# Optimization experiments

Hardware: AMD Instinct MI355X
Metric: run time of the kernel (lower is better)

## Reference

```python
import jax, jax.numpy as jnp
import numpy as np

CH = 50        # channel
RED = 2        # reduction -> match channels = 25
KS = 3         # ksize
SM_SCALE = 10.0
SCALES = [1.0, 0.9, 0.8, 0.7, 0.6]
ESCAPE_NAN = 1e-4


def prelu(x, a):
    return jnp.where(x >= 0, x, a * x)


def conv1x1(x, w, b):
    # x: [B,Ci,H,W], w: [Co,Ci], b: [Co]
    return jnp.einsum('bihw,oi->bohw', x, w) + b[None, :, None, None]


def patches3(x):
    # extract 3x3 stride-1 SAME patches, torch-unfold (C,kh,kw) ordering
    # x: [B,C,H,W] -> [B, H*W, C, 3, 3]
    B, C, H, W = x.shape
    p = jnp.pad(x, ((0, 0), (0, 0), (1, 1), (1, 1)))
    cols = jnp.stack([p[:, :, i:i + H, j:j + W]
                      for i in range(KS) for j in range(KS)], axis=2)  # [B,C,9,H,W]
    cols = cols.reshape(B, C, KS, KS, H * W)
    return cols.transpose(0, 4, 1, 2, 3)


def setup_inputs() -> dict:
    key = jax.random.key(0)
    ks = jax.random.split(key, 7)
    B, H, W = 4, 48, 48
    f = CH // RED  # 25
    s1 = 1.0 / np.sqrt(CH)
    return {
        'x': jax.random.normal(ks[0], (B, CH, H, W), jnp.float32),
        # conv_match_L_base: 1x1 conv CH->f + PReLU
        'w_base': jax.random.normal(ks[1], (f, CH), jnp.float32) * s1,
        'b_base': jnp.zeros((f,), jnp.float32),
        'a_base': jnp.float32(0.25),
        # conv_match: 1x1 conv CH->f + PReLU
        'w_match': jax.random.normal(ks[2], (f, CH), jnp.float32) * s1,
        'b_match': jnp.zeros((f,), jnp.float32),
        'a_match': jnp.float32(0.25),
        # conv_assembly: 1x1 conv CH->CH + PReLU
        'w_asm': jax.random.normal(ks[3], (CH, CH), jnp.float32) * s1,
        'b_asm': jnp.zeros((CH,), jnp.float32),
        'a_asm': jnp.float32(0.25),
    }


def reference(x, w_base, b_base, a_base, w_match, b_match, a_match,
              w_asm, b_asm, a_asm):
    B, C, H, W = x.shape
    match_base = prelu(conv1x1(x, w_base, b_base), a_base)  # [B,25,H,W]

    w_list, raw_list = [], []
    for s in SCALES:
        if s == 1.0:
            ref = x
        else:
            Hs, Ws = int(H * s), int(W * s)
            ref = jax.image.resize(x, (B, C, Hs, Ws), method='cubic')
        base = prelu(conv1x1(ref, w_asm, b_asm), a_asm)       # [B,C,Hs,Ws]
        raw_list.append(patches3(base))                       # [B,Hs*Ws,C,3,3]
        refm = prelu(conv1x1(ref, w_match, b_match), a_match)  # [B,25,Hs,Ws]
        w_list.append(patches3(refm))                         # [B,Hs*Ws,25,3,3]

    wi = jnp.concatenate(w_list, axis=1)    # [B, L, 25, 3, 3]
    raw = jnp.concatenate(raw_list, axis=1)  # [B, L, C, 3, 3]

    def attend(xb, wb, rb):
        # xb: [25,H,W]; wb: [L,25,3,3]; rb: [L,C,3,3]
        norm = jnp.maximum(
            jnp.sqrt(jnp.sum(wb * wb, axis=(1, 2, 3), keepdims=True)),
            ESCAPE_NAN)
        wn = wb / norm
        score = jax.lax.conv_general_dilated(
            xb[None], wn, (1, 1), [(1, 1), (1, 1)])[0]        # [L,H,W]
        attn = jax.nn.softmax(score * SM_SCALE, axis=0)
        # conv_transpose2d(stride=1, pad=1) == corr with flipped, transposed kernel
        wt = jnp.flip(rb, axis=(2, 3)).transpose(1, 0, 2, 3)  # [C,L,3,3]
        out = jax.lax.conv_general_dilated(
            attn[None], wt, (1, 1), [(1, 1), (1, 1)])[0]      # [C,H,W]
        return out * 0.25

    y = jax.vmap(attend)(match_base, wi, raw)
    return y + x  # res_scale = 1
```

## Files before the change

kernel.cpp:

```cpp
#include <hip/hip_runtime.h>
#include <hip/hip_bf16.h>
#include <math.h>


#define L_TOT 7470
#define L_PAD 7680
#define NCHUNK 4
#define CHUNK_TILES 30
#define KD    256
#define JD    512
#define HW    2304

typedef unsigned short u16;
typedef __attribute__((ext_vector_type(8))) short bf16x8;
typedef __attribute__((ext_vector_type(4))) float f32x4;

__device__ inline u16 f2b(float f) {
    __hip_bfloat16 h = __float2bfloat16(f);
    return __builtin_bit_cast(u16, h);
}
__device__ inline float b2f(u16 u) {
    __hip_bfloat16 h = __builtin_bit_cast(__hip_bfloat16, u);
    return __bfloat162float(h);
}

__constant__ int c_hs[5]   = {48, 43, 38, 33, 28};
__constant__ int c_loff[6] = {0, 2304, 4153, 5597, 6686, 7470};

__device__ inline void decode_l(int l, int& si, int& hs, int& pos) {
    si = 0;
#pragma unroll
    for (int s = 0; s < 4; ++s)
        if (l >= c_loff[s + 1]) si = s + 1;
    pos = l - c_loff[si];
    hs = c_hs[si];
}

#define GLOAD16(g, l) __builtin_amdgcn_global_load_lds(                          \
        (__attribute__((address_space(1))) const void*)(g),                      \
        (__attribute__((address_space(3))) void*)(l), 16, 0, 0)

__global__ void resize_weights_kernel(float* __restrict__ wmall) {
    int r = blockIdx.x * blockDim.x + threadIdx.x;
    if (r >= 142) return;
    int sizes[4] = {43, 38, 33, 28};
    int si = 0, i = r, woffs = 0;
    for (si = 0; si < 4; ++si) {
        if (i < sizes[si]) break;
        i -= sizes[si];
        woffs += sizes[si] * 48;
    }
    int osz = sizes[si];
    float inv_scale = 48.0f / (float)osz;
    float kscale = inv_scale;
    float sample_f = ((float)i + 0.5f) * inv_scale - 0.5f;
    float w[48];
    float tot = 0.f;
    for (int j = 0; j < 48; ++j) {
        float t = fabsf(sample_f - (float)j) / kscale;
        float v;
        if (t >= 2.f)       v = 0.f;
        else if (t >= 1.f)  v = ((-0.5f * t + 2.5f) * t - 4.f) * t + 2.f;
        else                v = ((1.5f * t - 2.5f) * t) * t + 1.f;
        w[j] = v;
        tot += v;
    }
    float invt = 1.f / tot;
    for (int j = 0; j < 48; ++j) wmall[woffs + i * 48 + j] = w[j] * invt;
}

__global__ void resize_h(const float* __restrict__ in, const float* __restrict__ wm,
                         float* __restrict__ tmp, int osz) {
    int idx = blockIdx.x * 256 + threadIdx.x;
    int total = 200 * osz * 48;
    if (idx >= total) return;
    int xi = idx % 48;
    int t = idx / 48;
    int yo = t % osz;
    int bc = t / osz;
    const float* wr = wm + yo * 48;
    const float* ip = in + (size_t)bc * 2304 + xi;
    float s = 0.f;
#pragma unroll
    for (int yi = 0; yi < 48; ++yi) s += wr[yi] * ip[yi * 48];
    tmp[idx] = s;
}

__global__ void resize_w(const float* __restrict__ tmp, const float* __restrict__ wm,
                         float* __restrict__ refout, int osz) {
    int idx = blockIdx.x * 256 + threadIdx.x;
    int total = 200 * osz * osz;
    if (idx >= total) return;
    int xo = idx % osz;
    int t = idx / osz;
    int yo = t % osz;
    int bc = t / osz;
    const float* wr = wm + xo * 48;
    const float* ip = tmp + ((size_t)bc * osz + yo) * 48;
    float s = 0.f;
#pragma unroll
    for (int xi = 0; xi < 48; ++xi) s += wr[xi] * ip[xi];
    refout[idx] = s;
}

__global__ void conv1x1_prelu(const float* __restrict__ in, const float* __restrict__ w,
                              const float* __restrict__ bias, const float* __restrict__ a,
                              float* __restrict__ outp, int P, int Co) {
    int idx = blockIdx.x * 256 + threadIdx.x;
    int total = 4 * Co * P;
    if (idx >= total) return;
    int p = idx % P;
    int t = idx / P;
    int co = t % Co;
    int b = t / Co;
    const float* ip = in + (size_t)b * 50 * P + p;
    const float* wr = w + co * 50;
    float s = bias[co];
#pragma unroll
    for (int ci = 0; ci < 50; ++ci) s += wr[ci] * ip[(size_t)ci * P];
    float av = a[0];
    outp[idx] = (s >= 0.f) ? s : av * s;
}

__global__ void q_build(const float* __restrict__ mb, u16* __restrict__ Q) {
    int idx = blockIdx.x * 256 + threadIdx.x;
    if (idx >= 4 * HW * KD) return;
    int k = idx % KD;
    int t = idx / KD;
    int p = t % HW;
    int b = t / HW;
    float v = 0.f;
    if (k < 225) {
        int c = k / 9, r = k % 9, ky = r / 3, kx = r % 3;
        int y = p / 48, xx = p % 48;
        int yy = y + ky - 1, xv = xx + kx - 1;
        if (yy >= 0 && yy < 48 && xv >= 0 && xv < 48)
            v = mb[((size_t)(b * 25 + c)) * HW + yy * 48 + xv];
    }
    Q[idx] = f2b(v);
}

__global__ void norms_kernel(const float* __restrict__ refm_all, float* __restrict__ norms) {
    int idx = blockIdx.x * 256 + threadIdx.x;
    if (idx >= 4 * L_TOT) return;
    int l = idx % L_TOT;
    int b = idx / L_TOT;
    int si, hs, pos;
    decode_l(l, si, hs, pos);
    int P = hs * hs;
    int ly = pos / hs, lx = pos % hs;
    const float* rb = refm_all + (size_t)100 * c_loff[si] + (size_t)(b * 25) * P;
    float ss = 0.f;
    for (int c = 0; c < 25; ++c) {
        const float* rc = rb + (size_t)c * P;
#pragma unroll
        for (int ky = 0; ky < 3; ++ky) {
#pragma unroll
            for (int kx = 0; kx < 3; ++kx) {
                int yy = ly + ky - 1, xv = lx + kx - 1;
                if (yy >= 0 && yy < hs && xv >= 0 && xv < hs) {
                    float v = rc[yy * hs + xv];
                    ss += v * v;
                }
            }
        }
    }
    norms[idx] = 10.0f / fmaxf(sqrtf(ss), 1e-4f);
}

__global__ void kt_build(const float* __restrict__ refm_all, const float* __restrict__ norms,
                         u16* __restrict__ K) {
    int idx = blockIdx.x * 256 + threadIdx.x;
    if (idx >= 4 * L_PAD * KD) return;
    int k = idx % KD;
    int t = idx / KD;
    int l = t % L_PAD;
    int b = t / L_PAD;
    float v = 0.f;
    if (k < 225 && l < L_TOT) {
        int si, hs, pos;
        decode_l(l, si, hs, pos);
        int P = hs * hs;
        int ly = pos / hs, lx = pos % hs;
        int c = k / 9, r = k % 9, ky = r / 3, kx = r % 3;
        int yy = ly + ky - 1, xv = lx + kx - 1;
        if (yy >= 0 && yy < hs && xv >= 0 && xv < hs)
            v = refm_all[(size_t)100 * c_loff[si] + ((size_t)(b * 25 + c)) * P + yy * hs + xv]
                * norms[(size_t)b * L_TOT + l];
    }
    K[idx] = f2b(v);
}

__global__ void v_build(const float* __restrict__ base_all, u16* __restrict__ VT) {
    int idx = blockIdx.x * 256 + threadIdx.x;
    if (idx >= 4 * JD * L_PAD) return;
    int l = idx % L_PAD;
    int t = idx / L_PAD;
    int j = t % JD;
    int b = t / JD;
    float v = 0.f;
    if (j < 450 && l < L_TOT) {
        int si, hs, pos;
        decode_l(l, si, hs, pos);
        int P = hs * hs;
        int ly = pos / hs, lx = pos % hs;
        int c = j / 9, r = j % 9, ky = r / 3, kx = r % 3;
        int yy = ly + ky - 1, xv = lx + kx - 1;
        if (yy >= 0 && yy < hs && xv >= 0 && xv < hs)
            v = base_all[(size_t)200 * c_loff[si] + ((size_t)(b * 50 + c)) * P + yy * hs + xv];
    }
    VT[idx] = f2b(v);
}

__global__ __launch_bounds__(256, 4) void attn_score(
    const u16* __restrict__ Qg, const u16* __restrict__ Kg,
    u16* __restrict__ Ag, float* __restrict__ mC, float* __restrict__ dC) {
    __shared__ u16 smem[64 * KD];
    __shared__ float sm_m[2][64], sm_d[2][64];
    const int bx = blockIdx.x, by = blockIdx.y;
    const int mt = by % 36, zq = by / 36;
    const int z16 = bx + 8 * zq;
    const int b = z16 >> 2, chunk = z16 & 3;
    const int bm = mt * 64;
    const u16* Q = Qg + (size_t)b * HW * KD;
    const u16* K = Kg + (size_t)b * L_PAD * KD;
    u16* A = Ag + (size_t)b * HW * L_PAD;
    const int tid = threadIdx.x, lane = tid & 63, wid = tid >> 6;
    const int wr = wid >> 1, wc = wid & 1;
    const int l15 = lane & 15, l16 = lane >> 4;
    const int l7 = lane & 7;
    const int r_lo = lane >> 5;
    const int u_dst = lane & 31;

    {
        const u16* qrow = Q + (size_t)(bm + wid * 16 + r_lo) * KD;
        u16* qdst = smem + (size_t)(wid * 16) * KD;
#pragma unroll
        for (int q = 0; q < 8; ++q) {
            int sw = (u_dst ^ ((q * 2 + r_lo) & 7)) * 8;
            GLOAD16(qrow + (size_t)(q * 2) * KD + sw, qdst + (q * 2) * KD);
        }
    }
    __syncthreads();
    bf16x8 qf[2][8];
#pragma unroll
    for (int m = 0; m < 2; ++m)
#pragma unroll
        for (int k = 0; k < 8; ++k)
            qf[m][k] = *(const bf16x8*)&smem[(size_t)(wr * 32 + m * 16 + l15) * KD
                                             + (((k * 4 + l16) ^ l7) * 8)];
    __syncthreads();

    float mrun[2][4];
#pragma unroll
    for (int m = 0; m < 2; ++m)
#pragma unroll
        for (int r = 0; r < 4; ++r) mrun[m][r] = -3e38f;

    const int t0 = chunk * CHUNK_TILES;
    const int colb_base = wc * 32 + l15;

    for (int t = t0; t < t0 + CHUNK_TILES; ++t) {
        {
            const u16* krow = K + (size_t)(t * 64 + wid * 16 + r_lo) * KD;
            u16* kdst = smem + (size_t)(wid * 16) * KD;
#pragma unroll
            for (int q = 0; q < 8; ++q) {
                int sw = (u_dst ^ ((q * 2 + r_lo) & 7)) * 8;
                GLOAD16(krow + (size_t)(q * 2) * KD + sw, kdst + (q * 2) * KD);
            }
        }
        __syncthreads();
        f32x4 acc[2][2];
#pragma unroll
        for (int m = 0; m < 2; ++m)
#pragma unroll
            for (int n = 0; n < 2; ++n) acc[m][n] = (f32x4){0.f, 0.f, 0.f, 0.f};
#pragma unroll
        for (int k = 0; k < 8; ++k) {
            bf16x8 bfr[2];
#pragma unroll
            for (int n = 0; n < 2; ++n)
                bfr[n] = *(const bf16x8*)&smem[(size_t)(wc * 32 + n * 16 + l15) * KD
                                               + (((k * 4 + l16) ^ l7) * 8)];
#pragma unroll
            for (int m = 0; m < 2; ++m)
#pragma unroll
                for (int n = 0; n < 2; ++n)
                    acc[m][n] = __builtin_amdgcn_mfma_f32_16x16x32_bf16(qf[m][k], bfr[n], acc[m][n], 0, 0, 0);
        }
        const int col0 = t * 64 + colb_base;
        const bool v0 = col0 < L_TOT, v1 = col0 + 16 < L_TOT;
#pragma unroll
        for (int m = 0; m < 2; ++m)
#pragma unroll
            for (int r = 0; r < 4; ++r) {
                float s0 = v0 ? acc[m][0][r] : -3e38f;
                float s1 = v1 ? acc[m][1][r] : -3e38f;
                mrun[m][r] = fmaxf(mrun[m][r], fmaxf(s0, s1));
            }
        __syncthreads();
    }

#pragma unroll
    for (int m = 0; m < 2; ++m)
#pragma unroll
        for (int r = 0; r < 4; ++r) {
            float mv = mrun[m][r];
#pragma unroll
            for (int st = 1; st <= 8; st <<= 1)
                mv = fmaxf(mv, __shfl_xor(mv, st));
            mrun[m][r] = mv;
        }
    if (l15 == 0) {
#pragma unroll
        for (int m = 0; m < 2; ++m)
#pragma unroll
            for (int r = 0; r < 4; ++r)
                sm_m[wc][wr * 32 + m * 16 + l16 * 4 + r] = mrun[m][r];
    }
    __syncthreads();
#pragma unroll
    for (int m = 0; m < 2; ++m)
#pragma unroll
        for (int r = 0; r < 4; ++r) {
            int row = wr * 32 + m * 16 + l16 * 4 + r;
            mrun[m][r] = fmaxf(sm_m[0][row], sm_m[1][row]);
        }

    float drun[2][4];
#pragma unroll
    for (int m = 0; m < 2; ++m)
#pragma unroll
        for (int r = 0; r < 4; ++r) drun[m][r] = 0.f;

    for (int t = t0; t < t0 + CHUNK_TILES; ++t) {
        {
            const u16* krow = K + (size_t)(t * 64 + wid * 16 + r_lo) * KD;
            u16* kdst = smem + (size_t)(wid * 16) * KD;
#pragma unroll
            for (int q = 0; q < 8; ++q) {
                int sw = (u_dst ^ ((q * 2 + r_lo) & 7)) * 8;
                GLOAD16(krow + (size_t)(q * 2) * KD + sw, kdst + (q * 2) * KD);
            }
        }
        __syncthreads();
        f32x4 acc[2][2];
#pragma unroll
        for (int m = 0; m < 2; ++m)
#pragma unroll
            for (int n = 0; n < 2; ++n) acc[m][n] = (f32x4){0.f, 0.f, 0.f, 0.f};
#pragma unroll
        for (int k = 0; k < 8; ++k) {
            bf16x8 bfr[2];
#pragma unroll
            for (int n = 0; n < 2; ++n)
                bfr[n] = *(const bf16x8*)&smem[(size_t)(wc * 32 + n * 16 + l15) * KD
                                               + (((k * 4 + l16) ^ l7) * 8)];
#pragma unroll
            for (int m = 0; m < 2; ++m)
#pragma unroll
                for (int n = 0; n < 2; ++n)
                    acc[m][n] = __builtin_amdgcn_mfma_f32_16x16x32_bf16(qf[m][k], bfr[n], acc[m][n], 0, 0, 0);
        }
        const int col0 = t * 64 + colb_base;
#pragma unroll
        for (int m = 0; m < 2; ++m) {
            const int row = bm + wr * 32 + m * 16 + l16 * 4;
#pragma unroll
            for (int n = 0; n < 2; ++n) {
                const int col = col0 + n * 16;
                const bool vld = col < L_TOT;
#pragma unroll
                for (int r = 0; r < 4; ++r) {
                    float w = vld ? __expf(acc[m][n][r] - mrun[m][r]) : 0.f;
                    drun[m][r] += w;
                    A[(size_t)(row + r) * L_PAD + col] = f2b(w);
                }
            }
        }
        __syncthreads();
    }

#pragma unroll
    for (int m = 0; m < 2; ++m)
#pragma unroll
        for (int r = 0; r < 4; ++r) {
            float dv = drun[m][r];
#pragma unroll
            for (int st = 1; st <= 8; st <<= 1)
                dv += __shfl_xor(dv, st);
            drun[m][r] = dv;
        }
    if (l15 == 0) {
#pragma unroll
        for (int m = 0; m < 2; ++m)
#pragma unroll
            for (int r = 0; r < 4; ++r)
                sm_d[wc][wr * 32 + m * 16 + l16 * 4 + r] = drun[m][r];
    }
    __syncthreads();
    if (wc == 0 && l15 == 0) {
#pragma unroll
        for (int m = 0; m < 2; ++m)
#pragma unroll
            for (int r = 0; r < 4; ++r) {
                int row = wr * 32 + m * 16 + l16 * 4 + r;
                size_t o = (size_t)(chunk * 4 + b) * HW + bm + row;
                mC[o] = mrun[m][r];
                dC[o] = sm_d[0][row] + sm_d[1][row];
            }
    }
}

__global__ void combine_stats(const float* __restrict__ mC, const float* __restrict__ dC,
                              float* __restrict__ fac) {
    int idx = blockIdx.x * 256 + threadIdx.x;
    if (idx >= 4 * HW) return;
    int b = idx / HW, p = idx % HW;
    float m[NCHUNK], d[NCHUNK];
#pragma unroll
    for (int c = 0; c < NCHUNK; ++c) {
        size_t o = (size_t)(c * 4 + b) * HW + p;
        m[c] = mC[o]; d[c] = dC[o];
    }
    float mf = m[0];
#pragma unroll
    for (int c = 1; c < NCHUNK; ++c) mf = fmaxf(mf, m[c]);
    float w[NCHUNK], df = 0.f;
#pragma unroll
    for (int c = 0; c < NCHUNK; ++c) { w[c] = __expf(m[c] - mf); df += d[c] * w[c]; }
    float inv = 1.0f / df;
#pragma unroll
    for (int c = 0; c < NCHUNK; ++c) fac[(size_t)(c * 4 + b) * HW + p] = w[c] * inv;
}

__global__ __launch_bounds__(256) void gemm2_kernel(
    const u16* __restrict__ VT0, const u16* __restrict__ A0, u16* __restrict__ C0) {
    __shared__ u16 As[128 * 64];
    __shared__ u16 Bs[128 * 64];
    const int bx = blockIdx.x, by = blockIdx.y;
    const int within = by % 72, zq = by / 72;
    const int mt = within & 3, nt = within >> 2;
    const int z = bx + 8 * zq;
    const int batch = z >> 2, chunk = z & 3;
    const u16* A = VT0 + (size_t)batch * JD * L_PAD + chunk * (CHUNK_TILES * 64);
    const u16* B = A0 + (size_t)batch * HW * L_PAD + chunk * (CHUNK_TILES * 64);
    u16* C = C0 + (size_t)z * JD * HW;
    const int bm = mt * 128, bn = nt * 128;
    const int tid = threadIdx.x, lane = tid & 63, wid = tid >> 6;
    const int wr = wid >> 1, wc = wid & 1;
    const int srow = lane >> 3;
    const int scol = (lane & 7) * 8;

    f32x4 acc[4][4];
#pragma unroll
    for (int i = 0; i < 4; ++i)
#pragma unroll
        for (int j = 0; j < 4; ++j) acc[i][j] = (f32x4){0.f, 0.f, 0.f, 0.f};

    const u16* aG = A + (size_t)(bm + wid * 32 + srow) * L_PAD + scol;
    const u16* bG = B + (size_t)(bn + wid * 32 + srow) * L_PAD + scol;
    u16* aL = As + wid * 32 * 64;
    u16* bL = Bs + wid * 32 * 64;

    for (int t = 0; t < CHUNK_TILES; ++t) {
#pragma unroll
        for (int q = 0; q < 4; ++q) {
            GLOAD16(aG + (size_t)q * 8 * L_PAD, aL + q * 8 * 64);
            GLOAD16(bG + (size_t)q * 8 * L_PAD, bL + q * 8 * 64);
        }
        aG += 64;
        bG += 64;
        __syncthreads();
#pragma unroll
        for (int kc = 0; kc < 64; kc += 32) {
            bf16x8 af[4], bf[4];
#pragma unroll
            for (int m = 0; m < 4; ++m)
                af[m] = *(const bf16x8*)&As[(wr * 64 + m * 16 + (lane & 15)) * 64 + kc + (lane >> 4) * 8];
#pragma unroll
            for (int n = 0; n < 4; ++n)
                bf[n] = *(const bf16x8*)&Bs[(wc * 64 + n * 16 + (lane & 15)) * 64 + kc + (lane >> 4) * 8];
#pragma unroll
            for (int m = 0; m < 4; ++m)
#pragma unroll
                for (int n = 0; n < 4; ++n)
                    acc[m][n] = __builtin_amdgcn_mfma_f32_16x16x32_bf16(af[m], bf[n], acc[m][n], 0, 0, 0);
        }
        __syncthreads();
    }
    const int crow0 = bm + wr * 64 + (lane >> 4) * 4;
    const int ccol = bn + wc * 64 + (lane & 15);
#pragma unroll
    for (int m = 0; m < 4; ++m)
#pragma unroll
        for (int n = 0; n < 4; ++n)
#pragma unroll
            for (int r = 0; r < 4; ++r)
                C[(size_t)(crow0 + m * 16 + r) * HW + ccol + n * 16] = f2b(acc[m][n][r]);
}

__global__ void chunk_reduce(const u16* __restrict__ Zt, const float* __restrict__ fac,
                             u16* __restrict__ Zred) {
    int idx = blockIdx.x * 256 + threadIdx.x;
    int total = 4 * JD * HW / 8;
    if (idx >= total) return;
    int e8 = idx * 8;
    int pp = e8 % HW;
    int row = e8 / HW;
    int b = row / JD;
    float s[8] = {};
#pragma unroll
    for (int ch = 0; ch < NCHUNK; ++ch) {
        const float* fp = fac + (size_t)(ch * 4 + b) * HW + pp;
        bf16x8 zv = *(const bf16x8*)&Zt[((size_t)(b * 4 + ch) * JD + (row % JD)) * HW + pp];
#pragma unroll
        for (int u = 0; u < 8; ++u)
            s[u] += fp[u] * b2f((u16)zv[u]);
    }
    bf16x8 o;
#pragma unroll
    for (int u = 0; u < 8; ++u) o[u] = (short)f2b(s[u]);
    *(bf16x8*)&Zred[(size_t)row * HW + pp] = o;
}

__global__ void final_kernel(const u16* __restrict__ Zred, const float* __restrict__ x,
                             float* __restrict__ out) {
    int idx = blockIdx.x * 256 + threadIdx.x;
    if (idx >= 4 * 50 * HW) return;
    int p = idx % HW;
    int t = idx / HW;
    int c = t % 50;
    int b = t / 50;
    int y = p / 48, xx = p % 48;
    const u16* Zb = Zred + (size_t)b * JD * HW;
    float s = 0.f;
#pragma unroll
    for (int ky = 0; ky < 3; ++ky) {
        int yy = y + ky - 1;
        if (yy < 0 || yy >= 48) continue;
#pragma unroll
        for (int kx = 0; kx < 3; ++kx) {
            int xv = xx + kx - 1;
            if (xv < 0 || xv >= 48) continue;
            int pp = yy * 48 + xv;
            int j = c * 9 + (2 - ky) * 3 + (2 - kx);
            s += b2f(Zb[(size_t)j * HW + pp]);
        }
    }
    size_t o = ((size_t)b * 50 + c) * HW + p;
    out[o] = x[o] + 0.25f * s;
}

extern "C" void kernel_launch(void* const* d_in, const int* in_sizes, int n_in,
                              void* d_out, int out_size, void* d_ws, size_t ws_size,
                              hipStream_t stream) {
    const float* x       = (const float*)d_in[0];
    const float* w_base  = (const float*)d_in[1];
    const float* b_base  = (const float*)d_in[2];
    const float* a_base  = (const float*)d_in[3];
    const float* w_match = (const float*)d_in[4];
    const float* b_match = (const float*)d_in[5];
    const float* a_match = (const float*)d_in[6];
    const float* w_asm   = (const float*)d_in[7];
    const float* b_asm   = (const float*)d_in[8];
    const float* a_asm   = (const float*)d_in[9];
    float* out = (float*)d_out;
    float* ws = (float*)d_ws;
    (void)in_sizes; (void)n_in; (void)out_size; (void)ws_size;

    const int hs[5] = {48, 43, 38, 33, 28};
    const int loff[6] = {0, 2304, 4153, 5597, 6686, 7470};

    size_t off = 0;
    auto alloc = [&](size_t n) { size_t o = off; off += (n + 63) & ~(size_t)63; return o; };
    size_t o_wm = alloc(142 * 48);
    size_t o_rtmp = alloc((size_t)200 * 43 * 48);
    size_t o_ref[5];
    o_ref[0] = 0;
    for (int si = 1; si < 5; ++si) o_ref[si] = alloc((size_t)200 * hs[si] * hs[si]);
    size_t o_base = alloc((size_t)200 * L_TOT);
    size_t o_refm = alloc((size_t)100 * L_TOT);
    size_t o_mb = alloc((size_t)100 * HW);
    size_t o_norms = alloc((size_t)4 * L_TOT);

    size_t o_A = 0;
    size_t o_Q = (size_t)4 * HW * L_PAD / 2;
    size_t o_K = o_Q + (size_t)4 * HW * KD / 2;
    size_t o_VT = o_K + (size_t)4 * L_PAD * KD / 2;
    size_t o_Z = o_VT + (size_t)4 * JD * L_PAD / 2;
    size_t o_mc = o_Z + (size_t)16 * JD * HW / 2;
    size_t o_dc = o_mc + (size_t)16 * HW;
    size_t o_fac = o_dc + (size_t)16 * HW;
    size_t o_zred = o_fac + (size_t)16 * HW;

    u16* Qb = (u16*)(ws + o_Q);
    u16* Kb = (u16*)(ws + o_K);
    u16* VTb = (u16*)(ws + o_VT);
    u16* Ab = (u16*)(ws + o_A);
    u16* Zb = (u16*)(ws + o_Z);
    u16* Zrb = (u16*)(ws + o_zred);

    resize_weights_kernel<<<1, 256, 0, stream>>>(ws + o_wm);
    const int woff[5] = {0, 0, 43 * 48, (43 + 38) * 48, (43 + 38 + 33) * 48};
    for (int si = 1; si < 5; ++si) {
        int osz = hs[si];
        int n1 = 200 * osz * 48;
        resize_h<<<(n1 + 255) / 256, 256, 0, stream>>>(x, ws + o_wm + woff[si], ws + o_rtmp, osz);
        int n2 = 200 * osz * osz;
        resize_w<<<(n2 + 255) / 256, 256, 0, stream>>>(ws + o_rtmp, ws + o_wm + woff[si],
                                                       ws + o_ref[si], osz);
    }
    for (int si = 0; si < 5; ++si) {
        int P = hs[si] * hs[si];
        const float* in = (si == 0) ? x : ws + o_ref[si];
        int nb = 4 * 50 * P;
        conv1x1_prelu<<<(nb + 255) / 256, 256, 0, stream>>>(
            in, w_asm, b_asm, a_asm, ws + o_base + (size_t)200 * loff[si], P, 50);
        int nm = 4 * 25 * P;
        conv1x1_prelu<<<(nm + 255) / 256, 256, 0, stream>>>(
            in, w_match, b_match, a_match, ws + o_refm + (size_t)100 * loff[si], P, 25);
    }
    {
        int nmb = 4 * 25 * HW;
        conv1x1_prelu<<<(nmb + 255) / 256, 256, 0, stream>>>(x, w_base, b_base, a_base,
                                                             ws + o_mb, HW, 25);
    }
    {
        int n = 4 * HW * KD;
        q_build<<<(n + 255) / 256, 256, 0, stream>>>(ws + o_mb, Qb);
    }
    {
        int n = 4 * L_TOT;
        norms_kernel<<<(n + 255) / 256, 256, 0, stream>>>(ws + o_refm, ws + o_norms);
    }
    {
        int n = 4 * L_PAD * KD;
        kt_build<<<(n + 255) / 256, 256, 0, stream>>>(ws + o_refm, ws + o_norms, Kb);
    }
    {
        int n = 4 * JD * L_PAD;
        v_build<<<(n + 255) / 256, 256, 0, stream>>>(ws + o_base, VTb);
    }

    {
        dim3 g(8, 72, 1);
        attn_score<<<g, 256, 0, stream>>>(Qb, Kb, Ab, ws + o_mc, ws + o_dc);
    }
    combine_stats<<<(4 * HW + 255) / 256, 256, 0, stream>>>(ws + o_mc, ws + o_dc, ws + o_fac);

    {
        dim3 g(8, 144, 1);
        gemm2_kernel<<<g, 256, 0, stream>>>(VTb, Ab, Zb);
    }
    {
        int n = 4 * JD * HW / 8;
        chunk_reduce<<<(n + 255) / 256, 256, 0, stream>>>(Zb, ws + o_fac, Zrb);
    }
    final_kernel<<<(4 * 50 * HW + 255) / 256, 256, 0, stream>>>(Zrb, x, out);
}
```

Before: 558.7 us.

## Merge preprocessing launches and restructure Q/K/V packing with a decode table

Collapses the per-scale resize and conv1x1 launches into single fused kernels (resize_h_all, resize_w_all, conv_all), cutting roughly twenty small launches to a few. A precomputed decode table replaces the per-element scale search. q_build and kt_build now have each thread write nine taps for one channel instead of one element. v_build writes eight bf16 values per thread with a vector store. This targets launch overhead and redundant index math in the preprocessing phase, at the cost of more branching and some uncoalesced scalar stores in the Q/K builders.

New measurement: 534.1 us. 1.05x faster.

```diff
diff --git a/kernel.cpp b/kernel.cpp
--- a/kernel.cpp
+++ b/kernel.cpp
@@ -27,134 +27,224 @@
 __constant__ int c_hs[5]   = {48, 43, 38, 33, 28};
 __constant__ int c_loff[6] = {0, 2304, 4153, 5597, 6686, 7470};
 
-__device__ inline void decode_l(int l, int& si, int& hs, int& pos) {
-    si = 0;
-#pragma unroll
-    for (int s = 0; s < 4; ++s)
-        if (l >= c_loff[s + 1]) si = s + 1;
-    pos = l - c_loff[si];
-    hs = c_hs[si];
-}
-
 #define GLOAD16(g, l) __builtin_amdgcn_global_load_lds(                          \
         (__attribute__((address_space(1))) const void*)(g),                      \
         (__attribute__((address_space(3))) void*)(l), 16, 0, 0)
 
-__global__ void resize_weights_kernel(float* __restrict__ wmall) {
-    int r = blockIdx.x * blockDim.x + threadIdx.x;
-    if (r >= 142) return;
-    int sizes[4] = {43, 38, 33, 28};
-    int si = 0, i = r, woffs = 0;
-    for (si = 0; si < 4; ++si) {
-        if (i < sizes[si]) break;
-        i -= sizes[si];
-        woffs += sizes[si] * 48;
-    }
-    int osz = sizes[si];
-    float inv_scale = 48.0f / (float)osz;
-    float kscale = inv_scale;
-    float sample_f = ((float)i + 0.5f) * inv_scale - 0.5f;
-    float w[48];
-    float tot = 0.f;
-    for (int j = 0; j < 48; ++j) {
-        float t = fabsf(sample_f - (float)j) / kscale;
-        float v;
-        if (t >= 2.f)       v = 0.f;
-        else if (t >= 1.f)  v = ((-0.5f * t + 2.5f) * t - 4.f) * t + 2.f;
-        else                v = ((1.5f * t - 2.5f) * t) * t + 1.f;
-        w[j] = v;
-        tot += v;
-    }
-    float invt = 1.f / tot;
-    for (int j = 0; j < 48; ++j) wmall[woffs + i * 48 + j] = w[j] * invt;
-}
-
-__global__ void resize_h(const float* __restrict__ in, const float* __restrict__ wm,
-                         float* __restrict__ tmp, int osz) {
-    int idx = blockIdx.x * 256 + threadIdx.x;
-    int total = 200 * osz * 48;
-    if (idx >= total) return;
-    int xi = idx % 48;
-    int t = idx / 48;
+__global__ void prep_kernel(float* __restrict__ wmall, int* __restrict__ dtab) {
+    int r = blockIdx.x * 256 + threadIdx.x;
+    if (r < 142) {
+        int sizes[4] = {43, 38, 33, 28};
+        int si = 0, i = r, woffs = 0;
+        for (si = 0; si < 4; ++si) {
+            if (i < sizes[si]) break;
+            i -= sizes[si];
+            woffs += sizes[si] * 48;
+        }
+        int osz = sizes[si];
+        float inv_scale = 48.0f / (float)osz;
+        float kscale = inv_scale;
+        float sample_f = ((float)i + 0.5f) * inv_scale - 0.5f;
+        float w[48];
+        float tot = 0.f;
+        for (int j = 0; j < 48; ++j) {
+            float t = fabsf(sample_f - (float)j) / kscale;
+            float v;
+            if (t >= 2.f)       v = 0.f;
+            else if (t >= 1.f)  v = ((-0.5f * t + 2.5f) * t - 4.f) * t + 2.f;
+            else                v = ((1.5f * t - 2.5f) * t) * t + 1.f;
+            w[j] = v;
+            tot += v;
+        }
+        float invt = 1.f / tot;
+        for (int j = 0; j < 48; ++j) wmall[woffs + i * 48 + j] = w[j] * invt;
+    }
+    if (r < L_PAD) {
+        int v;
+        if (r >= L_TOT) v = (int)0x80000000u;
+        else {
+            int si = 0;
+#pragma unroll
+            for (int s = 0; s < 4; ++s)
+                if (r >= c_loff[s + 1]) si = s + 1;
+            int pos = r - c_loff[si];
+            int hs = c_hs[si];
+            int ly = pos / hs, lx = pos % hs;
+            v = si | (ly << 4) | (lx << 10);
+        }
+        dtab[r] = v;
+    }
+}
+
+__global__ void resize_h_all(const float* __restrict__ in, const float* __restrict__ wm,
+                             float* __restrict__ t1, float* __restrict__ t2,
+                             float* __restrict__ t3, float* __restrict__ t4) {
+    int idx = blockIdx.x * 256 + threadIdx.x;
+    int rem = idx, osz, woffm;
+    float* tmp;
+    if (rem < 200 * 43 * 48) { osz = 43; tmp = t1; woffm = 0; }
+    else {
+        rem -= 200 * 43 * 48;
+        if (rem < 200 * 38 * 48) { osz = 38; tmp = t2; woffm = 43 * 48; }
+        else {
+            rem -= 200 * 38 * 48;
+            if (rem < 200 * 33 * 48) { osz = 33; tmp = t3; woffm = (43 + 38) * 48; }
+            else {
+                rem -= 200 * 33 * 48;
+                if (rem >= 200 * 28 * 48) return;
+                osz = 28; tmp = t4; woffm = (43 + 38 + 33) * 48;
+            }
+        }
+    }
+    int xi = rem % 48;
+    int t = rem / 48;
     int yo = t % osz;
     int bc = t / osz;
-    const float* wr = wm + yo * 48;
+    const float* wr = wm + (size_t)(woffm + yo * 48);
     const float* ip = in + (size_t)bc * 2304 + xi;
     float s = 0.f;
 #pragma unroll
     for (int yi = 0; yi < 48; ++yi) s += wr[yi] * ip[yi * 48];
-    tmp[idx] = s;
-}
-
-__global__ void resize_w(const float* __restrict__ tmp, const float* __restrict__ wm,
-                         float* __restrict__ refout, int osz) {
-    int idx = blockIdx.x * 256 + threadIdx.x;
-    int total = 200 * osz * osz;
-    if (idx >= total) return;
-    int xo = idx % osz;
-    int t = idx / osz;
+    tmp[rem] = s;
+}
+
+__global__ void resize_w_all(const float* __restrict__ t1, const float* __restrict__ t2,
+                             const float* __restrict__ t3, const float* __restrict__ t4,
+                             const float* __restrict__ wm,
+                             float* __restrict__ r1, float* __restrict__ r2,
+                             float* __restrict__ r3, float* __restrict__ r4) {
+    int idx = blockIdx.x * 256 + threadIdx.x;
+    int rem = idx, osz, woffm;
+    const float* tmp;
+    float* outp;
+    if (rem < 200 * 43 * 43) { osz = 43; tmp = t1; outp = r1; woffm = 0; }
+    else {
+        rem -= 200 * 43 * 43;
+        if (rem < 200 * 38 * 38) { osz = 38; tmp = t2; outp = r2; woffm = 43 * 48; }
+        else {
+            rem -= 200 * 38 * 38;
+            if (rem < 200 * 33 * 33) { osz = 33; tmp = t3; outp = r3; woffm = (43 + 38) * 48; }
+            else {
+                rem -= 200 * 33 * 33;
+                if (rem >= 200 * 28 * 28) return;
+                osz = 28; tmp = t4; outp = r4; woffm = (43 + 38 + 33) * 48;
+            }
+        }
+    }
+    int xo = rem % osz;
+    int t = rem / osz;
     int yo = t % osz;
     int bc = t / osz;
-    const float* wr = wm + xo * 48;
+    const float* wr = wm + (size_t)(woffm + xo * 48);
     const float* ip = tmp + ((size_t)bc * osz + yo) * 48;
     float s = 0.f;
 #pragma unroll
     for (int xi = 0; xi < 48; ++xi) s += wr[xi] * ip[xi];
-    refout[idx] = s;
-}
-
-__global__ void conv1x1_prelu(const float* __restrict__ in, const float* __restrict__ w,
-                              const float* __restrict__ bias, const float* __restrict__ a,
-                              float* __restrict__ outp, int P, int Co) {
-    int idx = blockIdx.x * 256 + threadIdx.x;
-    int total = 4 * Co * P;
-    if (idx >= total) return;
-    int p = idx % P;
-    int t = idx / P;
-    int co = t % Co;
-    int b = t / Co;
+    outp[rem] = s;
+}
+
+__global__ void conv_all(const float* __restrict__ x,
+                         const float* __restrict__ r1, const float* __restrict__ r2,
+                         const float* __restrict__ r3, const float* __restrict__ r4,
+                         const float* __restrict__ w_asm, const float* __restrict__ b_asm,
+                         const float* __restrict__ a_asm,
+                         const float* __restrict__ w_match, const float* __restrict__ b_match,
+                         const float* __restrict__ a_match,
+                         const float* __restrict__ w_base, const float* __restrict__ b_base,
+                         const float* __restrict__ a_base,
+                         float* __restrict__ base_out, float* __restrict__ refm_out,
+                         float* __restrict__ mb_out) {
+    int idx = blockIdx.x * 256 + threadIdx.x;
+    int rem = idx, P, loffv, NCO;
+    const float* in;
+    if (rem < 400 * 2304) { P = 2304; in = x; loffv = 0; NCO = 100; }
+    else {
+        rem -= 400 * 2304;
+        if (rem < 300 * 1849) { P = 1849; in = r1; loffv = 2304; NCO = 75; }
+        else {
+            rem -= 300 * 1849;
+            if (rem < 300 * 1444) { P = 1444; in = r2; loffv = 4153; NCO = 75; }
+            else {
+                rem -= 300 * 1444;
+                if (rem < 300 * 1089) { P = 1089; in = r3; loffv = 5597; NCO = 75; }
+                else {
+                    rem -= 300 * 1089;
+                    if (rem >= 300 * 784) return;
+                    P = 784; in = r4; loffv = 6686; NCO = 75;
+                }
+            }
+        }
+    }
+    int p = rem % P;
+    int t = rem / P;
+    int co = t % NCO;
+    int b = t / NCO;
     const float* ip = in + (size_t)b * 50 * P + p;
-    const float* wr = w + co * 50;
-    float s = bias[co];
+    const float* wr;
+    float bias, av;
+    float* outp;
+    if (co < 50) {
+        wr = w_asm + co * 50; bias = b_asm[co]; av = a_asm[0];
+        outp = base_out + (size_t)200 * loffv + ((size_t)(b * 50 + co)) * P + p;
+    } else if (co < 75) {
+        int cm = co - 50;
+        wr = w_match + cm * 50; bias = b_match[cm]; av = a_match[0];
+        outp = refm_out + (size_t)100 * loffv + ((size_t)(b * 25 + cm)) * P + p;
+    } else {
+        int cm = co - 75;
+        wr = w_base + cm * 50; bias = b_base[cm]; av = a_base[0];
+        outp = mb_out + ((size_t)(b * 25 + cm)) * P + p;
+    }
+    float s = bias;
 #pragma unroll
     for (int ci = 0; ci < 50; ++ci) s += wr[ci] * ip[(size_t)ci * P];
-    float av = a[0];
-    outp[idx] = (s >= 0.f) ? s : av * s;
+    *outp = (s >= 0.f) ? s : av * s;
 }
 
 __global__ void q_build(const float* __restrict__ mb, u16* __restrict__ Q) {
     int idx = blockIdx.x * 256 + threadIdx.x;
-    if (idx >= 4 * HW * KD) return;
-    int k = idx % KD;
-    int t = idx / KD;
+    if (idx >= 4 * HW * 25) return;
+    int c = idx % 25;
+    int t = idx / 25;
     int p = t % HW;
     int b = t / HW;
-    float v = 0.f;
-    if (k < 225) {
-        int c = k / 9, r = k % 9, ky = r / 3, kx = r % 3;
-        int y = p / 48, xx = p % 48;
-        int yy = y + ky - 1, xv = xx + kx - 1;
-        if (yy >= 0 && yy < 48 && xv >= 0 && xv < 48)
-            v = mb[((size_t)(b * 25 + c)) * HW + yy * 48 + xv];
-    }
-    Q[idx] = f2b(v);
-}
-
-__global__ void norms_kernel(const float* __restrict__ refm_all, float* __restrict__ norms) {
-    int idx = blockIdx.x * 256 + threadIdx.x;
-    if (idx >= 4 * L_TOT) return;
-    int l = idx % L_TOT;
-    int b = idx / L_TOT;
-    int si, hs, pos;
-    decode_l(l, si, hs, pos);
-    int P = hs * hs;
-    int ly = pos / hs, lx = pos % hs;
+    int y = p / 48, xx = p % 48;
+    const float* rc = mb + (size_t)(b * 25 + c) * HW;
+    u16 ov[9];
+#pragma unroll
+    for (int ky = 0; ky < 3; ++ky)
+#pragma unroll
+        for (int kx = 0; kx < 3; ++kx) {
+            int yy = y + ky - 1, xv = xx + kx - 1;
+            float v = (yy >= 0 && yy < 48 && xv >= 0 && xv < 48) ? rc[yy * 48 + xv] : 0.f;
+            ov[ky * 3 + kx] = f2b(v);
+        }
+    u16* dst = Q + (size_t)(b * HW + p) * KD + c * 9;
+#pragma unroll
+    for (int r = 0; r < 9; ++r) dst[r] = ov[r];
+    if (c == 24) {
+        u16* z = dst + 9;
+#pragma unroll
+        for (int i = 0; i < 31; ++i) z[i] = 0;
+    }
+}
+
+__global__ void norms_kernel(const float* __restrict__ refm_all, const int* __restrict__ dtab,
+                             float* __restrict__ norms) {
+    int idx = blockIdx.x * 256 + threadIdx.x;
+    if (idx >= 4 * L_PAD) return;
+    int l = idx % L_PAD;
+    int b = idx / L_PAD;
+    int d = dtab[l];
+    if (d < 0) return;
+    int si = d & 15, ly = (d >> 4) & 63, lx = (d >> 10) & 63;
+    int hs = c_hs[si], P = hs * hs;
     const float* rb = refm_all + (size_t)100 * c_loff[si] + (size_t)(b * 25) * P;
     float ss = 0.f;
     for (int c = 0; c < 25; ++c) {
         const float* rc = rb + (size_t)c * P;
 #pragma unroll
-        for (int ky = 0; ky < 3; ++ky) {
+        for (int ky = 0; ky < 3; ++ky)
 #pragma unroll
             for (int kx = 0; kx < 3; ++kx) {
                 int yy = ly + ky - 1, xv = lx + kx - 1;
@@ -163,53 +253,71 @@
                     ss += v * v;
                 }
             }
-        }
-    }
-    norms[idx] = 10.0f / fmaxf(sqrtf(ss), 1e-4f);
-}
-
-__global__ void kt_build(const float* __restrict__ refm_all, const float* __restrict__ norms,
-                         u16* __restrict__ K) {
-    int idx = blockIdx.x * 256 + threadIdx.x;
-    if (idx >= 4 * L_PAD * KD) return;
-    int k = idx % KD;
-    int t = idx / KD;
+    }
+    norms[(size_t)b * L_PAD + l] = 10.0f / fmaxf(sqrtf(ss), 1e-4f);
+}
+
+__global__ void kt_build(const float* __restrict__ refm_all, const int* __restrict__ dtab,
+                         const float* __restrict__ norms, u16* __restrict__ K) {
+    int idx = blockIdx.x * 256 + threadIdx.x;
+    if (idx >= 4 * L_PAD * 25) return;
+    int c = idx % 25;
+    int t = idx / 25;
     int l = t % L_PAD;
     int b = t / L_PAD;
-    float v = 0.f;
-    if (k < 225 && l < L_TOT) {
-        int si, hs, pos;
-        decode_l(l, si, hs, pos);
-        int P = hs * hs;
-        int ly = pos / hs, lx = pos % hs;
-        int c = k / 9, r = k % 9, ky = r / 3, kx = r % 3;
-        int yy = ly + ky - 1, xv = lx + kx - 1;
-        if (yy >= 0 && yy < hs && xv >= 0 && xv < hs)
-            v = refm_all[(size_t)100 * c_loff[si] + ((size_t)(b * 25 + c)) * P + yy * hs + xv]
-                * norms[(size_t)b * L_TOT + l];
-    }
-    K[idx] = f2b(v);
-}
-
-__global__ void v_build(const float* __restrict__ base_all, u16* __restrict__ VT) {
-    int idx = blockIdx.x * 256 + threadIdx.x;
-    if (idx >= 4 * JD * L_PAD) return;
-    int l = idx % L_PAD;
-    int t = idx / L_PAD;
+    u16 ov[9] = {0, 0, 0, 0, 0, 0, 0, 0, 0};
+    int d = dtab[l];
+    if (d >= 0) {
+        int si = d & 15, ly = (d >> 4) & 63, lx = (d >> 10) & 63;
+        int hs = c_hs[si], P = hs * hs;
+        float nrm = norms[(size_t)b * L_PAD + l];
+        const float* rc = refm_all + (size_t)100 * c_loff[si] + (size_t)(b * 25 + c) * P;
+#pragma unroll
+        for (int ky = 0; ky < 3; ++ky)
+#pragma unroll
+            for (int kx = 0; kx < 3; ++kx) {
+                int yy = ly + ky - 1, xv = lx + kx - 1;
+                if (yy >= 0 && yy < hs && xv >= 0 && xv < hs)
+                    ov[ky * 3 + kx] = f2b(rc[yy * hs + xv] * nrm);
+            }
+    }
+    u16* dst = K + (size_t)(b * L_PAD + l) * KD + c * 9;
+#pragma unroll
+    for (int r = 0; r < 9; ++r) dst[r] = ov[r];
+    if (c == 24) {
+        u16* z = dst + 9;
+#pragma unroll
+        for (int i = 0; i < 31; ++i) z[i] = 0;
+    }
+}
+
+__global__ void v_build(const float* __restrict__ base_all, const int* __restrict__ dtab,
+                        u16* __restrict__ VT) {
+    int idx = blockIdx.x * 256 + threadIdx.x;
+    if (idx >= 4 * JD * (L_PAD / 8)) return;
+    int l8 = idx % (L_PAD / 8);
+    int t = idx / (L_PAD / 8);
     int j = t % JD;
     int b = t / JD;
-    float v = 0.f;
-    if (j < 450 && l < L_TOT) {
-        int si, hs, pos;
-        decode_l(l, si, hs, pos);
-        int P = hs * hs;
-        int ly = pos / hs, lx = pos % hs;
+    int l0 = l8 * 8;
+    bf16x8 ov = (bf16x8){0, 0, 0, 0, 0, 0, 0, 0};
+    if (j < 450) {
         int c = j / 9, r = j % 9, ky = r / 3, kx = r % 3;
-        int yy = ly + ky - 1, xv = lx + kx - 1;
-        if (yy >= 0 && yy < hs && xv >= 0 && xv < hs)
-            v = base_all[(size_t)200 * c_loff[si] + ((size_t)(b * 50 + c)) * P + yy * hs + xv];
-    }
-    VT[idx] = f2b(v);
+#pragma unroll
+        for (int u = 0; u < 8; ++u) {
+            int d = dtab[l0 + u];
+            float v = 0.f;
+            if (d >= 0) {
+                int si = d & 15, ly = (d >> 4) & 63, lx = (d >> 10) & 63;
+                int hs = c_hs[si], P = hs * hs;
+                int yy = ly + ky - 1, xv = lx + kx - 1;
+                if (yy >= 0 && yy < hs && xv >= 0 && xv < hs)
+                    v = base_all[(size_t)200 * c_loff[si] + (size_t)(b * 50 + c) * P + yy * hs + xv];
+            }
+            ov[u] = (short)f2b(v);
+        }
+    }
+    *(bf16x8*)&VT[(size_t)(b * JD + j) * L_PAD + l0] = ov;
 }
 
 __global__ __launch_bounds__(256, 4) void attn_score(
@@ -570,20 +678,22 @@
     float* ws = (float*)d_ws;
     (void)in_sizes; (void)n_in; (void)out_size; (void)ws_size;
 
-    const int hs[5] = {48, 43, 38, 33, 28};
-    const int loff[6] = {0, 2304, 4153, 5597, 6686, 7470};
-
     size_t off = 0;
     auto alloc = [&](size_t n) { size_t o = off; off += (n + 63) & ~(size_t)63; return o; };
     size_t o_wm = alloc(142 * 48);
-    size_t o_rtmp = alloc((size_t)200 * 43 * 48);
-    size_t o_ref[5];
-    o_ref[0] = 0;
-    for (int si = 1; si < 5; ++si) o_ref[si] = alloc((size_t)200 * hs[si] * hs[si]);
+    size_t o_dtab = alloc(L_PAD);
+    size_t o_t1 = alloc((size_t)200 * 43 * 48);
+    size_t o_t2 = alloc((size_t)200 * 38 * 48);
+    size_t o_t3 = alloc((size_t)200 * 33 * 48);
+    size_t o_t4 = alloc((size_t)200 * 28 * 48);
+    size_t o_r1 = alloc((size_t)200 * 43 * 43);
+    size_t o_r2 = alloc((size_t)200 * 38 * 38);
+    size_t o_r3 = alloc((size_t)200 * 33 * 33);
+    size_t o_r4 = alloc((size_t)200 * 28 * 28);
     size_t o_base = alloc((size_t)200 * L_TOT);
     size_t o_refm = alloc((size_t)100 * L_TOT);
     size_t o_mb = alloc((size_t)100 * HW);
-    size_t o_norms = alloc((size_t)4 * L_TOT);
+    size_t o_norms = alloc((size_t)4 * L_PAD);
 
     size_t o_A = 0;
     size_t o_Q = (size_t)4 * HW * L_PAD / 2;
@@ -601,47 +711,42 @@
     u16* Ab = (u16*)(ws + o_A);
     u16* Zb = (u16*)(ws + o_Z);
     u16* Zrb = (u16*)(ws + o_zred);
-
-    resize_weights_kernel<<<1, 256, 0, stream>>>(ws + o_wm);
-    const int woff[5] = {0, 0, 43 * 48, (43 + 38) * 48, (43 + 38 + 33) * 48};
-    for (int si = 1; si < 5; ++si) {
-        int osz = hs[si];
-        int n1 = 200 * osz * 48;
-        resize_h<<<(n1 + 255) / 256, 256, 0, stream>>>(x, ws + o_wm + woff[si], ws + o_rtmp, osz);
-        int n2 = 200 * osz * osz;
-        resize_w<<<(n2 + 255) / 256, 256, 0, stream>>>(ws + o_rtmp, ws + o_wm + woff[si],
-                                                       ws + o_ref[si], osz);
-    }
-    for (int si = 0; si < 5; ++si) {
-        int P = hs[si] * hs[si];
-        const float* in = (si == 0) ? x : ws + o_ref[si];
-        int nb = 4 * 50 * P;
-        conv1x1_prelu<<<(nb + 255) / 256, 256, 0, stream>>>(
-            in, w_asm, b_asm, a_asm, ws + o_base + (size_t)200 * loff[si], P, 50);
-        int nm = 4 * 25 * P;
-        conv1x1_prelu<<<(nm + 255) / 256, 256, 0, stream>>>(
-            in, w_match, b_match, a_match, ws + o_refm + (size_t)100 * loff[si], P, 25);
-    }
-    {
-        int nmb = 4 * 25 * HW;
-        conv1x1_prelu<<<(nmb + 255) / 256, 256, 0, stream>>>(x, w_base, b_base, a_base,
-                                                             ws + o_mb, HW, 25);
-    }
-    {
-        int n = 4 * HW * KD;
+    int* dtab = (int*)(ws + o_dtab);
+
+    prep_kernel<<<(L_PAD + 255) / 256, 256, 0, stream>>>(ws + o_wm, dtab);
+    {
+        int n = 200 * 48 * (43 + 38 + 33 + 28);
+        resize_h_all<<<(n + 255) / 256, 256, 0, stream>>>(x, ws + o_wm, ws + o_t1,
+                                                          ws + o_t2, ws + o_t3, ws + o_t4);
+    }
+    {
+        int n = 200 * (43 * 43 + 38 * 38 + 33 * 33 + 28 * 28);
+        resize_w_all<<<(n + 255) / 256, 256, 0, stream>>>(ws + o_t1, ws + o_t2, ws + o_t3,
+                                                          ws + o_t4, ws + o_wm, ws + o_r1,
+                                                          ws + o_r2, ws + o_r3, ws + o_r4);
+    }
+    {
+        int n = 400 * 2304 + 300 * (1849 + 1444 + 1089 + 784);
+        conv_all<<<(n + 255) / 256, 256, 0, stream>>>(
+            x, ws + o_r1, ws + o_r2, ws + o_r3, ws + o_r4,
+            w_asm, b_asm, a_asm, w_match, b_match, a_match, w_base, b_base, a_base,
+            ws + o_base, ws + o_refm, ws + o_mb);
+    }
+    {
+        int n = 4 * HW * 25;
         q_build<<<(n + 255) / 256, 256, 0, stream>>>(ws + o_mb, Qb);
     }
     {
-        int n = 4 * L_TOT;
-        norms_kernel<<<(n + 255) / 256, 256, 0, stream>>>(ws + o_refm, ws + o_norms);
-    }
-    {
-        int n = 4 * L_PAD * KD;
-        kt_build<<<(n + 255) / 256, 256, 0, stream>>>(ws + o_refm, ws + o_norms, Kb);
-    }
-    {
-        int n = 4 * JD * L_PAD;
-        v_build<<<(n + 255) / 256, 256, 0, stream>>>(ws + o_base, VTb);
+        int n = 4 * L_PAD;
+        norms_kernel<<<(n + 255) / 256, 256, 0, stream>>>(ws + o_refm, dtab, ws + o_norms);
+    }
+    {
+        int n = 4 * L_PAD * 25;
+        kt_build<<<(n + 255) / 256, 256, 0, stream>>>(ws + o_refm, dtab, ws + o_norms, Kb);
+    }
+    {
+        int n = 4 * JD * (L_PAD / 8);
+        v_build<<<(n + 255) / 256, 256, 0, stream>>>(ws + o_base, dtab, VTb);
     }
 
     {
```
